# Kernel optimization log

Hardware: AMD Instinct MI355X
Metric: run time of the kernel (lower is better)

Reference implementation:

```python
import jax, jax.numpy as jnp
import numpy as np

SEQ, D_IN, D_OUT = 4096, 768, 768

def setup_inputs() -> dict:
    key = jax.random.key(0)
    kx, kq, kk, kv = jax.random.split(key, 4)
    s = 1.0 / np.sqrt(D_IN)
    return {
        "x": jax.random.normal(kx, (SEQ, D_IN), dtype=jnp.float32),
        "Wq": jax.random.uniform(kq, (D_IN, D_OUT), jnp.float32, -s, s),
        "Wk": jax.random.uniform(kk, (D_IN, D_OUT), jnp.float32, -s, s),
        "Wv": jax.random.uniform(kv, (D_IN, D_OUT), jnp.float32, -s, s),
    }

def reference(x, Wq, Wk, Wv):
    # x: [S, d_in]; Wq/Wk/Wv: [d_in, d_out] (torch nn.Linear weight transposed)
    q = x @ Wq
    k = x @ Wk
    v = x @ Wv
    scores = (q @ k.T) / jnp.sqrt(jnp.asarray(k.shape[1], q.dtype))  # [S, S]
    weights = jax.nn.softmax(scores, axis=1)
    return weights @ v  # [S, d_out]
```

## Files before the change

### kernel.cpp

```cpp
#include <hip/hip_runtime.h>
#include <hip/hip_bf16.h>

typedef __bf16 bf16x8 __attribute__((ext_vector_type(8)));
typedef float  f32x4  __attribute__((ext_vector_type(4)));
typedef float  f4     __attribute__((ext_vector_type(4)));
typedef unsigned short us4 __attribute__((ext_vector_type(4)));
typedef unsigned short us8 __attribute__((ext_vector_type(8)));

__device__ inline unsigned short f2bf(float f) {
  union { float f; unsigned int u; } v; v.f = f;
  unsigned int r = v.u + 0x7fffu + ((v.u >> 16) & 1u);
  return (unsigned short)(r >> 16);
}
__device__ inline float bf2f(unsigned short u) {
  union { unsigned int u; float f; } v; v.u = (unsigned int)u << 16;
  return v.f;
}

__device__ inline void gload_lds16(const void* g, void* l) {
  __builtin_amdgcn_global_load_lds((const __attribute__((address_space(1))) void*)g,
                                   (__attribute__((address_space(3))) void*)l, 16, 0, 0);
}

__global__ __launch_bounds__(256) void convfused(const float* __restrict__ x,
                                                 const float* __restrict__ Wq,
                                                 const float* __restrict__ Wk,
                                                 const float* __restrict__ Wv,
                                                 unsigned short* __restrict__ xb,
                                                 unsigned short* __restrict__ wt) {
  __shared__ unsigned short tile[32][33];
  if (blockIdx.x < 3072) {
    int i = blockIdx.x * 256 + threadIdx.x;
    f4 v = ((const f4*)x)[i];
    us4 o;
    #pragma unroll
    for (int c = 0; c < 4; ++c) o[c] = f2bf(v[c]);
    ((us4*)xb)[i] = o;
  } else {
    int b = blockIdx.x - 3072;
    int bz = b / 576, rem = b % 576;
    int bx = rem / 24, by = rem % 24;
    const float* W = bz == 0 ? Wq : (bz == 1 ? Wk : Wv);
    int k0 = bx * 32, n0 = by * 32;
    int c = threadIdx.x & 31, r8 = threadIdx.x >> 5;
    #pragma unroll
    for (int p = 0; p < 4; ++p) {
      int r = p * 8 + r8;
      tile[r][c] = f2bf(W[(size_t)(k0 + r) * 768 + n0 + c]);
    }
    __syncthreads();
    #pragma unroll
    for (int p = 0; p < 4; ++p) {
      int r = p * 8 + r8;
      wt[((size_t)bz * 768 + n0 + r) * 768 + k0 + c] = tile[c][r];
    }
  }
}

template <int WAVES, int WM, int WN, int MINW, typename OUT_T, bool DOEXP, bool DOSCALE, bool UNI>
__global__ __launch_bounds__(WAVES * 64, MINW) void gemmdp(const unsigned short* __restrict__ A,
                                                           const unsigned short* __restrict__ B,
                                                           OUT_T* __restrict__ C0,
                                                           OUT_T* __restrict__ C1,
                                                           const float* __restrict__ rowinv,
                                                           const unsigned short* __restrict__ A2,
                                                           const unsigned short* __restrict__ B2,
                                                           OUT_T* __restrict__ C2,
                                                           int lda, int ldb, int ldc, int nbx,
                                                           int lda2, int ldb2, int ldc2, int nbx2,
                                                           int nsplit, int kspan, float cscale) {
  constexpr int BM = WAVES * 32, BN = WAVES * 32;
  constexpr int MF = 2 * WAVES / WM, NF = 2 * WAVES / WN;
  constexpr int SLOT = (BM + BN) * 64;
  __shared__ __align__(16) char lds[4 * SLOT];
  const int tid = threadIdx.x;
  const int w = tid >> 6, l = tid & 63;
  const int wr = w / WN, wc = w % WN;
  const int lr = l & 15, lk = l >> 4;

  const int nwg = gridDim.x;
  const int swz = (blockIdx.x & 7) * (nwg >> 3) + (blockIdx.x >> 3);

  const unsigned short* Ap = A;
  const unsigned short* Bp = B;
  OUT_T* Cp = blockIdx.y ? C1 : C0;
  int LDA = lda, LDB = ldb, LDC = ldc;
  int bx, by;
  if constexpr (UNI) {
    if (swz < nsplit) { bx = swz % nbx;  by = swz / nbx; }
    else {
      int s2 = swz - nsplit;
      bx = s2 % nbx2; by = s2 / nbx2;
      Ap = A2; Bp = B2; Cp = C2; LDA = lda2; LDB = ldb2; LDC = ldc2;
    }
  } else {
    bx = swz % nbx; by = swz / nbx;
  }
  const int m0 = by * BM, n0 = bx * BN;
  const int koff0 = blockIdx.y * kspan;

  f32x4 acc[MF][NF] = {};

  const int trow = tid >> 2;
  const int koff = ((tid & 3) * 8) ^ (((tid >> 5) & 1) * 16);
  const unsigned short* gA0 = Ap + (size_t)(m0 + trow) * LDA + koff + koff0;
  const unsigned short* gA1 = Ap + (size_t)(m0 + BM / 2 + trow) * LDA + koff + koff0;
  const unsigned short* gB0 = Bp + (size_t)(n0 + trow) * LDB + koff + koff0;
  const unsigned short* gB1 = Bp + (size_t)(n0 + BN / 2 + trow) * LDB + koff + koff0;
  const int wave16 = (tid & ~63) * 16;

  auto stage = [&](int slot, int k0) {
    char* base = lds + slot * SLOT;
    gload_lds16(gA0 + k0, base + wave16);
    gload_lds16(gA1 + k0, base + BM * 32 + wave16);
    gload_lds16(gB0 + k0, base + BM * 64 + wave16);
    gload_lds16(gB1 + k0, base + BM * 64 + BN * 32 + wave16);
  };

  const int xorv = ((l >> 3) & 1) << 5;
  const int aoff = (wr * (MF * 16) + lr) * 64 + lk * 16;
  const int boff = BM * 64 + (wc * (NF * 16) + lr) * 64 + lk * 16;

  auto ldfrags = [&](int slot, bf16x8 (&pa)[MF], bf16x8 (&pb)[NF]) {
    const char* sb = lds + slot * SLOT;
    #pragma unroll
    for (int mf = 0; mf < MF; ++mf)
      pa[mf] = *(const bf16x8*)(sb + ((aoff + mf * 1024) ^ xorv));
    #pragma unroll
    for (int nf = 0; nf < NF; ++nf)
      pb[nf] = *(const bf16x8*)(sb + ((boff + nf * 1024) ^ xorv));
  };

  const int nsteps = kspan >> 5;
  bf16x8 fa[MF], fb[NF], ga[MF], gb[NF];

  stage(0, 0); stage(1, 32); stage(2, 64);
  asm volatile("s_waitcnt vmcnt(8)" ::: "memory");
  __builtin_amdgcn_s_barrier();
  ldfrags(0, fa, fb);

  auto step = [&](int s, bf16x8 (&ca)[MF], bf16x8 (&cb)[NF],
                  bf16x8 (&xa)[MF], bf16x8 (&xb2)[NF]) {
    __builtin_amdgcn_sched_barrier(0);
    if (s < nsteps - 2) asm volatile("s_waitcnt vmcnt(4)" ::: "memory");
    else                asm volatile("s_waitcnt vmcnt(0)" ::: "memory");
    __builtin_amdgcn_s_barrier();
    __builtin_amdgcn_sched_barrier(0);

    if (s + 3 < nsteps) stage((s + 3) & 3, (s + 3) << 5);
    if (s + 1 < nsteps) ldfrags((s + 1) & 3, xa, xb2);

    __builtin_amdgcn_s_setprio(1);
    #pragma unroll
    for (int mf = 0; mf < MF; ++mf)
      #pragma unroll
      for (int nf = 0; nf < NF; ++nf)
        acc[mf][nf] = __builtin_amdgcn_mfma_f32_16x16x32_bf16(ca[mf], cb[nf], acc[mf][nf], 0, 0, 0);
    __builtin_amdgcn_s_setprio(0);
  };

  for (int s = 0; s < nsteps; s += 2) {
    step(s,     fa, fb, ga, gb);
    step(s + 1, ga, gb, fa, fb);
  }

  #pragma unroll
  for (int mf = 0; mf < MF; ++mf)
    #pragma unroll
    for (int nf = 0; nf < NF; ++nf)
      #pragma unroll
      for (int i = 0; i < 4; ++i) {
        int r = m0 + wr * (MF * 16) + mf * 16 + lk * 4 + i;
        int c = n0 + wc * (NF * 16) + nf * 16 + lr;
        float v = acc[mf][nf][i] * cscale;
        if constexpr (DOEXP)   v = __expf(v);
        if constexpr (DOSCALE) v *= rowinv[r];
        if constexpr (__is_same(OUT_T, unsigned short)) Cp[(size_t)r * LDC + c] = f2bf(v);
        else                                            Cp[(size_t)r * LDC + c] = v;
      }
}

__global__ __launch_bounds__(256) void rowsum(const unsigned short* __restrict__ P,
                                              float* __restrict__ rowinv) {
  const int wv = threadIdx.x >> 6, l = threadIdx.x & 63;
  const int r = blockIdx.x * 4 + wv;
  const unsigned short* row = P + (size_t)r * 4096;
  float sum = 0.f;
  #pragma unroll
  for (int j = 0; j < 8; ++j) {
    us8 v = ((const us8*)row)[l + j * 64];
    #pragma unroll
    for (int c = 0; c < 8; ++c) sum += bf2f(v[c]);
  }
  #pragma unroll
  for (int o = 32; o > 0; o >>= 1) sum += __shfl_xor(sum, o);
  if (l == 0) rowinv[r] = 1.f / sum;
}

__global__ __launch_bounds__(256) void reduce_add(float* __restrict__ out,
                                                  const float* __restrict__ p1) {
  int i = blockIdx.x * 256 + threadIdx.x;
  f4 a = ((const f4*)out)[i];
  f4 b = ((const f4*)p1)[i];
  #pragma unroll
  for (int c = 0; c < 4; ++c) a[c] += b[c];
  ((f4*)out)[i] = a;
}

extern "C" void kernel_launch(void* const* d_in, const int* in_sizes, int n_in,
                              void* d_out, int out_size, void* d_ws, size_t ws_size,
                              hipStream_t stream) {
  const float* x  = (const float*)d_in[0];
  const float* Wq = (const float*)d_in[1];
  const float* Wk = (const float*)d_in[2];
  const float* Wv = (const float*)d_in[3];
  float* out = (float*)d_out;
  char* ws = (char*)d_ws;

  unsigned short* qkv = (unsigned short*)ws;
  unsigned short* P   = (unsigned short*)(ws + 18874368);
  unsigned short* xb  = (unsigned short*)(ws + 18874368);
  unsigned short* wt  = (unsigned short*)(ws + 18874368 + 6291456);
  unsigned short* vt  = (unsigned short*)(ws + 52428800);
  float* rowinvp      = (float*)(ws + 58720256);
  float* p1           = (float*)ws;

  const float qscale = 0.03608439182435161f;

  convfused<<<4800, 256, 0, stream>>>(x, Wq, Wk, Wv, xb, wt);
  gemmdp<4, 2, 2, 2, unsigned short, false, false, true><<<576, 256, 0, stream>>>(
      xb, wt, qkv, qkv, nullptr,
      wt + (size_t)1536 * 768, xb, vt,
      768, 768, 1536, 12,
      768, 768, 4096, 32,
      384, 768, 1.0f);
  gemmdp<8, 2, 4, 2, unsigned short, true, false, false><<<256, 512, 0, stream>>>(
      qkv, qkv + 768, P, P, nullptr, nullptr, nullptr, nullptr,
      1536, 1536, 4096, 16, 0, 0, 0, 0, 0, 768, qscale);
  rowsum<<<1024, 256, 0, stream>>>(P, rowinvp);
  gemmdp<4, 2, 2, 2, float, false, true, false><<<dim3(192, 2), 256, 0, stream>>>(
      P, vt, out, p1, rowinvp, nullptr, nullptr, nullptr,
      4096, 4096, 768, 6, 0, 0, 0, 0, 0, 2048, 1.0f);
  reduce_add<<<3072, 256, 0, stream>>>(out, p1);
}
```

Measured before the change: 114.8 us.

## Fuse softmax row-sum partials into the QK^T exp GEMM epilogue

The exp GEMM now computes per-row partial sums of the exponentiated scores in registers, reduces them across lanes with shuffles, and writes one partial per column group. A tiny kernel then sums the 64 partials per row into the inverse row sum. This replaces the separate rowsum pass that re-read the whole 4096x4096 bf16 P matrix. The exp GEMM also switches from the 8-wave, 256-block configuration to the 4-wave, 1024-block one, which changes tile shape and occupancy. The partial sums are taken from fp32 values rather than from the bf16-rounded P, so the normalisation differs slightly from before.

```diff
diff --git a/kernel.cpp b/kernel.cpp
--- a/kernel.cpp
+++ b/kernel.cpp
@@ -11,10 +11,6 @@
   union { float f; unsigned int u; } v; v.f = f;
   unsigned int r = v.u + 0x7fffu + ((v.u >> 16) & 1u);
   return (unsigned short)(r >> 16);
-}
-__device__ inline float bf2f(unsigned short u) {
-  union { unsigned int u; float f; } v; v.u = (unsigned int)u << 16;
-  return v.f;
 }
 
 __device__ inline void gload_lds16(const void* g, void* l) {
@@ -57,12 +53,14 @@
   }
 }
 
-template <int WAVES, int WM, int WN, int MINW, typename OUT_T, bool DOEXP, bool DOSCALE, bool UNI>
+template <int WAVES, int WM, int WN, int MINW, typename OUT_T,
+          bool DOEXP, bool DOSCALE, bool UNI, bool PSUM>
 __global__ __launch_bounds__(WAVES * 64, MINW) void gemmdp(const unsigned short* __restrict__ A,
                                                            const unsigned short* __restrict__ B,
                                                            OUT_T* __restrict__ C0,
                                                            OUT_T* __restrict__ C1,
                                                            const float* __restrict__ rowinv,
+                                                           float* __restrict__ psum,
                                                            const unsigned short* __restrict__ A2,
                                                            const unsigned short* __restrict__ B2,
                                                            OUT_T* __restrict__ C2,
@@ -164,6 +162,16 @@
     step(s + 1, ga, gb, fa, fb);
   }
 
+  if constexpr (DOEXP) {
+    #pragma unroll
+    for (int mf = 0; mf < MF; ++mf)
+      #pragma unroll
+      for (int nf = 0; nf < NF; ++nf)
+        #pragma unroll
+        for (int i = 0; i < 4; ++i)
+          acc[mf][nf][i] = __expf(acc[mf][nf][i] * cscale);
+  }
+
   #pragma unroll
   for (int mf = 0; mf < MF; ++mf)
     #pragma unroll
@@ -172,29 +180,41 @@
       for (int i = 0; i < 4; ++i) {
         int r = m0 + wr * (MF * 16) + mf * 16 + lk * 4 + i;
         int c = n0 + wc * (NF * 16) + nf * 16 + lr;
-        float v = acc[mf][nf][i] * cscale;
-        if constexpr (DOEXP)   v = __expf(v);
+        float v = acc[mf][nf][i];
+        if constexpr (!DOEXP) v *= cscale;
         if constexpr (DOSCALE) v *= rowinv[r];
         if constexpr (__is_same(OUT_T, unsigned short)) Cp[(size_t)r * LDC + c] = f2bf(v);
         else                                            Cp[(size_t)r * LDC + c] = v;
       }
-}
-
-__global__ __launch_bounds__(256) void rowsum(const unsigned short* __restrict__ P,
-                                              float* __restrict__ rowinv) {
-  const int wv = threadIdx.x >> 6, l = threadIdx.x & 63;
-  const int r = blockIdx.x * 4 + wv;
-  const unsigned short* row = P + (size_t)r * 4096;
-  float sum = 0.f;
+
+  if constexpr (PSUM) {
+    const int cg = bx * WN + wc;
+    #pragma unroll
+    for (int mf = 0; mf < MF; ++mf)
+      #pragma unroll
+      for (int i = 0; i < 4; ++i) {
+        float rp = 0.f;
+        #pragma unroll
+        for (int nf = 0; nf < NF; ++nf) rp += acc[mf][nf][i];
+        rp += __shfl_xor(rp, 1);
+        rp += __shfl_xor(rp, 2);
+        rp += __shfl_xor(rp, 4);
+        rp += __shfl_xor(rp, 8);
+        if (lr == 0) {
+          int r = m0 + wr * (MF * 16) + mf * 16 + lk * 4 + i;
+          psum[(size_t)cg * 4096 + r] = rp;
+        }
+      }
+  }
+}
+
+__global__ __launch_bounds__(256) void rowinvk(const float* __restrict__ psum,
+                                               float* __restrict__ rowinv) {
+  int r = blockIdx.x * 256 + threadIdx.x;
+  float s = 0.f;
   #pragma unroll
-  for (int j = 0; j < 8; ++j) {
-    us8 v = ((const us8*)row)[l + j * 64];
-    #pragma unroll
-    for (int c = 0; c < 8; ++c) sum += bf2f(v[c]);
-  }
-  #pragma unroll
-  for (int o = 32; o > 0; o >>= 1) sum += __shfl_xor(sum, o);
-  if (l == 0) rowinv[r] = 1.f / sum;
+  for (int cg = 0; cg < 64; ++cg) s += psum[(size_t)cg * 4096 + r];
+  rowinv[r] = 1.f / s;
 }
 
 __global__ __launch_bounds__(256) void reduce_add(float* __restrict__ out,
@@ -223,23 +243,24 @@
   unsigned short* wt  = (unsigned short*)(ws + 18874368 + 6291456);
   unsigned short* vt  = (unsigned short*)(ws + 52428800);
   float* rowinvp      = (float*)(ws + 58720256);
+  float* psum         = (float*)(ws + 58736640);
   float* p1           = (float*)ws;
 
   const float qscale = 0.03608439182435161f;
 
   convfused<<<4800, 256, 0, stream>>>(x, Wq, Wk, Wv, xb, wt);
-  gemmdp<4, 2, 2, 2, unsigned short, false, false, true><<<576, 256, 0, stream>>>(
-      xb, wt, qkv, qkv, nullptr,
+  gemmdp<4, 2, 2, 2, unsigned short, false, false, true, false><<<576, 256, 0, stream>>>(
+      xb, wt, qkv, qkv, nullptr, nullptr,
       wt + (size_t)1536 * 768, xb, vt,
       768, 768, 1536, 12,
       768, 768, 4096, 32,
       384, 768, 1.0f);
-  gemmdp<8, 2, 4, 2, unsigned short, true, false, false><<<256, 512, 0, stream>>>(
-      qkv, qkv + 768, P, P, nullptr, nullptr, nullptr, nullptr,
-      1536, 1536, 4096, 16, 0, 0, 0, 0, 0, 768, qscale);
-  rowsum<<<1024, 256, 0, stream>>>(P, rowinvp);
-  gemmdp<4, 2, 2, 2, float, false, true, false><<<dim3(192, 2), 256, 0, stream>>>(
-      P, vt, out, p1, rowinvp, nullptr, nullptr, nullptr,
+  gemmdp<4, 2, 2, 2, unsigned short, true, false, false, true><<<1024, 256, 0, stream>>>(
+      qkv, qkv + 768, P, P, nullptr, psum, nullptr, nullptr, nullptr,
+      1536, 1536, 4096, 32, 0, 0, 0, 0, 0, 768, qscale);
+  rowinvk<<<16, 256, 0, stream>>>(psum, rowinvp);
+  gemmdp<4, 2, 2, 2, float, false, true, false, false><<<dim3(192, 2), 256, 0, stream>>>(
+      P, vt, out, p1, rowinvp, nullptr, nullptr, nullptr, nullptr,
       4096, 4096, 768, 6, 0, 0, 0, 0, 0, 2048, 1.0f);
   reduce_add<<<3072, 256, 0, stream>>>(out, p1);
 }
```

Result: slower. 140.3 us (+22.2%).
